# Performance work log

Hardware: AMD Instinct MI355X
Metric: run time of the kernel (lower is better)

The kernel has to match this reference:

```python
import jax, jax.numpy as jnp
import numpy as np

# DeepSeek-MoE-like sizes
T, H, I, E = 4096, 4096, 1408, 16  # tokens, hidden, intermediate, experts
TPE = T // E  # tokens per expert (equal, contiguous groups)


def setup_inputs() -> dict:
    key = jax.random.key(0)
    ks = jax.random.split(key, 5)
    x = jax.random.normal(ks[0], (T, H), dtype=jnp.float32)
    # int8 weights (stored as int8, accumulated in int32)
    w13 = jax.random.randint(ks[1], (E, 2 * I, H), -127, 128, dtype=jnp.int32).astype(jnp.int8)
    w2 = jax.random.randint(ks[2], (E, H, I), -127, 128, dtype=jnp.int32).astype(jnp.int8)
    # per-expert per-output-channel dequant scales (small, realistic magnitudes)
    w13_scale = jax.random.uniform(ks[3], (E, 2 * I), minval=1e-4, maxval=2e-4, dtype=jnp.float32)
    smooth_scale_2 = jnp.ones((E, I), dtype=jnp.float32)
    w2_scale = jax.random.uniform(ks[4], (E, H), minval=1e-4, maxval=2e-4, dtype=jnp.float32)
    # group_list_type=0: cumulative token counts per expert (equal contiguous groups)
    expert_tokens = jnp.cumsum(jnp.full((E,), TPE, dtype=jnp.int32))
    return {"x": x, "w13": w13, "w2": w2, "w13_scale": w13_scale,
            "smooth_scale_2": smooth_scale_2, "w2_scale": w2_scale,
            "expert_tokens": expert_tokens}


def _dynamic_quant(x):
    # per-token symmetric int8 dynamic quantization (npu_dynamic_quant)
    scale = jnp.max(jnp.abs(x), axis=-1, keepdims=True) / 127.0  # [T,1]
    q = jnp.clip(jnp.round(x / scale), -128, 127).astype(jnp.int8)
    return q, scale


def reference(x, w13, w2, w13_scale, smooth_scale_2, w2_scale, expert_tokens):
    # expert_tokens is the cumulative group list; this reference assumes the
    # equal contiguous grouping produced by setup_inputs (TPE tokens/expert).
    del expert_tokens
    # 1) per-token dynamic quant of activations
    xq, s1 = _dynamic_quant(x)                       # int8 [T,H], f32 [T,1]
    xg = xq.reshape(E, TPE, H).astype(jnp.int32)
    s1 = s1.reshape(E, TPE, 1)
    # 2) grouped int8 GEMM -> int32 (w1||w3 fused)
    mm1 = jnp.einsum('eth,eoh->eto', xg, w13.astype(jnp.int32))  # int32 [E,TPE,2I]
    # 3) fused dequant + SwiGLU (activate_left) + smooth-scale + dynamic requant
    y = mm1.astype(jnp.float32) * w13_scale[:, None, :] * s1
    gate, up = y[..., :I], y[..., I:]
    h = jax.nn.silu(gate) * up                        # f32 [E,TPE,I]
    h = h * smooth_scale_2[:, None, :]
    s2 = jnp.max(jnp.abs(h), axis=-1, keepdims=True) / 127.0
    hq = jnp.clip(jnp.round(h / s2), -128, 127).astype(jnp.int32)
    # 4) grouped int8 GEMM with fused per-channel + per-token dequant
    mm2 = jnp.einsum('eti,ehi->eth', hq, w2.astype(jnp.int32))   # int32 [E,TPE,H]
    out = mm2.astype(jnp.float32) * w2_scale[:, None, :] * s2
    return out.reshape(T, H)
```

## Files before the change

### kernel.cpp

```cpp
#include <hip/hip_runtime.h>
#include <stdint.h>

#define T_TOK 4096
#define H_DIM 4096
#define I_DIM 1408
#define E_NUM 16
#define TPE   256

typedef __attribute__((ext_vector_type(4))) int   i32x4;
typedef __attribute__((ext_vector_type(4))) float f32x4;

#define VMCNT(n) asm volatile("s_waitcnt vmcnt(" #n ")" ::: "memory")
#define LGKM0()  asm volatile("s_waitcnt lgkmcnt(0)" ::: "memory")

__device__ __forceinline__ void gload16(const void* g, void* l) {
  __builtin_amdgcn_global_load_lds(
      (const __attribute__((address_space(1))) void*)g,
      (__attribute__((address_space(3))) void*)l, 16, 0, 0);
}

__global__ __launch_bounds__(256)
void quant_x_kernel(const float* __restrict__ x,
                    int8_t* __restrict__ xq,
                    float* __restrict__ s1) {
  const int t   = blockIdx.x;
  const int tid = threadIdx.x;
  const float* row = x + (size_t)t * H_DIM;

  f32x4 v[4];
  float mx = 0.0f;
#pragma unroll
  for (int i = 0; i < 4; ++i) {
    v[i] = *(const f32x4*)(row + (size_t)(i * 256 + tid) * 4);
#pragma unroll
    for (int j = 0; j < 4; ++j) mx = fmaxf(mx, fabsf(v[i][j]));
  }
#pragma unroll
  for (int off = 32; off > 0; off >>= 1) mx = fmaxf(mx, __shfl_xor(mx, off));
  __shared__ float wmax[4];
  if ((tid & 63) == 0) wmax[tid >> 6] = mx;
  __syncthreads();
  float s = fmaxf(fmaxf(wmax[0], wmax[1]), fmaxf(wmax[2], wmax[3])) / 127.0f;
  s = fmaxf(s, 1e-30f);

  int* orow = (int*)(xq + (size_t)t * H_DIM);
#pragma unroll
  for (int i = 0; i < 4; ++i) {
    int packed = 0;
#pragma unroll
    for (int j = 0; j < 4; ++j) {
      float q = rintf(v[i][j] / s);
      q = fminf(fmaxf(q, -128.0f), 127.0f);
      packed |= ((int)q & 0xff) << (8 * j);
    }
    orow[i * 256 + tid] = packed;
  }
  if (tid == 0) s1[t] = s;
}

__global__ __launch_bounds__(256)
void act_quant_kernel(const float* __restrict__ y,
                      const float* __restrict__ smooth,
                      int8_t* __restrict__ hq,
                      float* __restrict__ s2) {
  const int t   = blockIdx.x;
  const int e   = t >> 8;
  const int tid = threadIdx.x;
  const float* gate = y + (size_t)t * (2 * I_DIM);
  const float* up   = gate + I_DIM;
  const float* ss   = smooth + (size_t)e * I_DIM;
  constexpr int NV = I_DIM / 4;

  f32x4 h[2];
  float mx = 0.0f;
#pragma unroll
  for (int i = 0; i < 2; ++i) {
    const int idx = tid + i * 256;
    h[i] = (f32x4)(0.0f);
    if (idx < NV) {
      const f32x4 g4 = *(const f32x4*)(gate + idx * 4);
      const f32x4 u4 = *(const f32x4*)(up + idx * 4);
      const f32x4 s4 = *(const f32x4*)(ss + idx * 4);
#pragma unroll
      for (int j = 0; j < 4; ++j) {
        const float g = g4[j];
        const float sig = 1.0f / (1.0f + expf(-g));
        h[i][j] = ((g * sig) * u4[j]) * s4[j];
        mx = fmaxf(mx, fabsf(h[i][j]));
      }
    }
  }
#pragma unroll
  for (int off = 32; off > 0; off >>= 1) mx = fmaxf(mx, __shfl_xor(mx, off));
  __shared__ float wmax[4];
  if ((tid & 63) == 0) wmax[tid >> 6] = mx;
  __syncthreads();
  float s = fmaxf(fmaxf(wmax[0], wmax[1]), fmaxf(wmax[2], wmax[3])) / 127.0f;
  s = fmaxf(s, 1e-30f);

  int* orow = (int*)(hq + (size_t)t * I_DIM);
#pragma unroll
  for (int i = 0; i < 2; ++i) {
    const int idx = tid + i * 256;
    if (idx < NV) {
      int packed = 0;
#pragma unroll
      for (int j = 0; j < 4; ++j) {
        float q = rintf(h[i][j] / s);
        q = fminf(fmaxf(q, -128.0f), 127.0f);
        packed |= ((int)q & 0xff) << (8 * j);
      }
      orow[idx] = packed;
    }
  }
  if (tid == 0) s2[t] = s;
}

template <int N, int K, int NBLK>
__global__ __launch_bounds__(512, 4)
void gemm_i8_w32_kernel(const int8_t* __restrict__ A,
                        const int* __restrict__ B32,
                        float* __restrict__ C,
                        const float* __restrict__ scaleN,
                        const float* __restrict__ scaleM) {
  constexpr int NT = K / 128;
  __shared__ __align__(16) int8_t As[2][256 * 128];
  __shared__ __align__(16) int8_t Bs[2][64 * 128];

  const int rid  = blockIdx.x;
  const int xcd  = rid & 7;
  const int slot = rid >> 3;
  const int el   = (slot >= NBLK) ? 1 : 0;
  const int e    = 2 * xcd + el;
  const int bn   = slot - el * NBLK;

  const int tid  = threadIdx.x;
  const int lane = tid & 63;
  const int wid  = tid >> 6;
  const int wm   = wid >> 1;
  const int wn   = wid & 1;

  const int8_t* Abase = A + (size_t)e * TPE * K;
  const int*    Bbase = B32 + ((size_t)e * N + (size_t)bn * 64) * (size_t)K;

  const int arow = tid >> 3;
  const int ablk = tid & 7;
  const int akey = arow & 7;
  const int agblk = ablk ^ akey;
  const int8_t* gA[4];
#pragma unroll
  for (int i = 0; i < 4; ++i)
    gA[i] = Abase + (size_t)(arow + 64 * i) * K + (agblk << 4);

  const int brow = tid >> 3;
  const int bblk = tid & 7;
  const int* gB = Bbase + (size_t)brow * K + (bblk << 4);
  const int bldsOff = brow * 128 + ((bblk ^ (brow & 7)) << 4);

  const int r15 = lane & 15;
  const int kg  = lane >> 4;
  int aoff[2][4], boff[2][2];
#pragma unroll
  for (int ks = 0; ks < 2; ++ks) {
#pragma unroll
    for (int m = 0; m < 4; ++m) {
      const int r = wm * 64 + m * 16 + r15;
      aoff[ks][m] = r * 128 + (((ks * 4 + kg) ^ (r & 7)) << 4);
    }
#pragma unroll
    for (int n = 0; n < 2; ++n) {
      const int r = wn * 32 + n * 16 + r15;
      boff[ks][n] = r * 128 + (((ks * 4 + kg) ^ (r & 7)) << 4);
    }
  }

  i32x4 acc[4][2] = {};
  i32x4 n0, n1, n2, n3;

  {
    i32x4 b0 = *(const i32x4*)(gB + 0);
    i32x4 b1 = *(const i32x4*)(gB + 4);
    i32x4 b2 = *(const i32x4*)(gB + 8);
    i32x4 b3 = *(const i32x4*)(gB + 12);
#pragma unroll
    for (int i = 0; i < 4; ++i)
      gload16(gA[i], &As[0][i * 8192 + wid * 1024]);
    VMCNT(4);
    i32x4 pk;
    pk[0] = (b0[0] & 255) | ((b0[1] & 255) << 8) | ((b0[2] & 255) << 16) | (b0[3] << 24);
    pk[1] = (b1[0] & 255) | ((b1[1] & 255) << 8) | ((b1[2] & 255) << 16) | (b1[3] << 24);
    pk[2] = (b2[0] & 255) | ((b2[1] & 255) << 8) | ((b2[2] & 255) << 16) | (b2[3] << 24);
    pk[3] = (b3[0] & 255) | ((b3[1] & 255) << 8) | ((b3[2] & 255) << 16) | (b3[3] << 24);
    *(i32x4*)(&Bs[0][bldsOff]) = pk;
    if (NT > 1) {
      const int* g = gB + 128;
      n0 = *(const i32x4*)(g + 0);
      n1 = *(const i32x4*)(g + 4);
      n2 = *(const i32x4*)(g + 8);
      n3 = *(const i32x4*)(g + 12);
      VMCNT(4);
    } else {
      VMCNT(0);
    }
    LGKM0();
    __builtin_amdgcn_s_barrier();
  }

  for (int t = 0; t < NT; ++t) {
    const int cur = t & 1;
    if (t + 1 < NT) {
      const size_t ko = (size_t)(t + 1) * 128;
#pragma unroll
      for (int i = 0; i < 4; ++i)
        gload16(gA[i] + ko, &As[cur ^ 1][i * 8192 + wid * 1024]);
    }
#pragma unroll
    for (int ks = 0; ks < 2; ++ks) {
      i32x4 av[4], bv[2];
#pragma unroll
      for (int m = 0; m < 4; ++m) av[m] = *(const i32x4*)(&As[cur][aoff[ks][m]]);
#pragma unroll
      for (int n = 0; n < 2; ++n) bv[n] = *(const i32x4*)(&Bs[cur][boff[ks][n]]);
#pragma unroll
      for (int m = 0; m < 4; ++m)
#pragma unroll
        for (int n = 0; n < 2; ++n)
          acc[m][n] = __builtin_amdgcn_mfma_i32_16x16x64_i8(av[m], bv[n], acc[m][n], 0, 0, 0);
    }
    if (t + 1 < NT) {
      VMCNT(4);
      i32x4 pk;
      pk[0] = (n0[0] & 255) | ((n0[1] & 255) << 8) | ((n0[2] & 255) << 16) | (n0[3] << 24);
      pk[1] = (n1[0] & 255) | ((n1[1] & 255) << 8) | ((n1[2] & 255) << 16) | (n1[3] << 24);
      pk[2] = (n2[0] & 255) | ((n2[1] & 255) << 8) | ((n2[2] & 255) << 16) | (n2[3] << 24);
      pk[3] = (n3[0] & 255) | ((n3[1] & 255) << 8) | ((n3[2] & 255) << 16) | (n3[3] << 24);
      *(i32x4*)(&Bs[cur ^ 1][bldsOff]) = pk;
      if (t + 2 < NT) {
        const int* g = gB + (t + 2) * 128;
        n0 = *(const i32x4*)(g + 0);
        n1 = *(const i32x4*)(g + 4);
        n2 = *(const i32x4*)(g + 8);
        n3 = *(const i32x4*)(g + 12);
        VMCNT(4);
      } else {
        VMCNT(0);
      }
      LGKM0();
      __builtin_amdgcn_s_barrier();
    }
  }

  const float* sN = scaleN + (size_t)e * N + (size_t)bn * 64;
  const float* sM = scaleM + e * TPE;
  float* Cbase = C + (size_t)e * TPE * N + (size_t)bn * 64;
#pragma unroll
  for (int m = 0; m < 4; ++m) {
#pragma unroll
    for (int j = 0; j < 4; ++j) {
      const int row = wm * 64 + m * 16 + kg * 4 + j;
      const float smv = sM[row];
      float* cr = Cbase + (size_t)row * N;
#pragma unroll
      for (int n = 0; n < 2; ++n) {
        const int col = wn * 32 + n * 16 + r15;
        cr[col] = ((float)acc[m][n][j] * sN[col]) * smv;
      }
    }
  }
}

extern "C" void kernel_launch(void* const* d_in, const int* in_sizes, int n_in,
                              void* d_out, int out_size, void* d_ws, size_t ws_size,
                              hipStream_t stream) {
  const float* x         = (const float*)d_in[0];
  const int*   w13       = (const int*)d_in[1];
  const int*   w2        = (const int*)d_in[2];
  const float* w13_scale = (const float*)d_in[3];
  const float* smooth    = (const float*)d_in[4];
  const float* w2_scale  = (const float*)d_in[5];

  uint8_t* ws = (uint8_t*)d_ws;
  int8_t* xq = (int8_t*)ws;
  int8_t* hq = (int8_t*)ws;
  float*  s1 = (float*)(ws + 16777216);
  float*  s2 = (float*)(ws + 16777216 + 16384);
  float*  y  = (float*)(ws + 16777216 + 32768);

  float* out = (float*)d_out;

  quant_x_kernel<<<dim3(T_TOK), dim3(256), 0, stream>>>(x, xq, s1);

  gemm_i8_w32_kernel<2 * I_DIM, H_DIM, 44>
      <<<dim3(8 * 2 * 44), dim3(512), 0, stream>>>(
          xq, w13, y, w13_scale, s1);

  act_quant_kernel<<<dim3(T_TOK), dim3(256), 0, stream>>>(y, smooth, hq, s2);

  gemm_i8_w32_kernel<H_DIM, I_DIM, 64>
      <<<dim3(8 * 2 * 64), dim3(512), 0, stream>>>(
          hq, w2, out, w2_scale, s2);
}
```

Measured before the change: 282.8 us.

## Fuse SwiGLU and smooth-scale into GEMM1 epilogue with atomic row max

GEMM1 tiles now pair 32 gate columns with the matching 32 up columns, so the epilogue can dequantize, apply SiLU*up and the smooth scale, and write h (T x I floats) rather than y (T x 2I floats). The per-token absmax is accumulated with a 16-lane shuffle reduction plus an atomicMax on the float bit pattern into a buffer that quant_x_kernel zeroes. A light pack kernel then only quantizes h. This removes half of the intermediate write and read traffic and the separate activation pass, at the cost of global atomics and transcendental work in the GEMM epilogue.

After: 286.4 us. Within noise of the previous version (+1.3%).

```diff
diff --git a/kernel.cpp b/kernel.cpp
--- a/kernel.cpp
+++ b/kernel.cpp
@@ -22,7 +22,8 @@
 __global__ __launch_bounds__(256)
 void quant_x_kernel(const float* __restrict__ x,
                     int8_t* __restrict__ xq,
-                    float* __restrict__ s1) {
+                    float* __restrict__ s1,
+                    unsigned* __restrict__ s2max) {
   const int t   = blockIdx.x;
   const int tid = threadIdx.x;
   const float* row = x + (size_t)t * H_DIM;
@@ -55,84 +56,60 @@
     }
     orow[i * 256 + tid] = packed;
   }
-  if (tid == 0) s1[t] = s;
+  if (tid == 0) { s1[t] = s; s2max[t] = 0u; }
 }
 
 __global__ __launch_bounds__(256)
-void act_quant_kernel(const float* __restrict__ y,
-                      const float* __restrict__ smooth,
-                      int8_t* __restrict__ hq,
-                      float* __restrict__ s2) {
+void act_pack_kernel(const float* __restrict__ h,
+                     const unsigned* __restrict__ s2max,
+                     int8_t* __restrict__ hq,
+                     float* __restrict__ s2) {
   const int t   = blockIdx.x;
-  const int e   = t >> 8;
   const int tid = threadIdx.x;
-  const float* gate = y + (size_t)t * (2 * I_DIM);
-  const float* up   = gate + I_DIM;
-  const float* ss   = smooth + (size_t)e * I_DIM;
   constexpr int NV = I_DIM / 4;
-
-  f32x4 h[2];
-  float mx = 0.0f;
-#pragma unroll
-  for (int i = 0; i < 2; ++i) {
-    const int idx = tid + i * 256;
-    h[i] = (f32x4)(0.0f);
-    if (idx < NV) {
-      const f32x4 g4 = *(const f32x4*)(gate + idx * 4);
-      const f32x4 u4 = *(const f32x4*)(up + idx * 4);
-      const f32x4 s4 = *(const f32x4*)(ss + idx * 4);
-#pragma unroll
-      for (int j = 0; j < 4; ++j) {
-        const float g = g4[j];
-        const float sig = 1.0f / (1.0f + expf(-g));
-        h[i][j] = ((g * sig) * u4[j]) * s4[j];
-        mx = fmaxf(mx, fabsf(h[i][j]));
-      }
-    }
-  }
-#pragma unroll
-  for (int off = 32; off > 0; off >>= 1) mx = fmaxf(mx, __shfl_xor(mx, off));
-  __shared__ float wmax[4];
-  if ((tid & 63) == 0) wmax[tid >> 6] = mx;
-  __syncthreads();
-  float s = fmaxf(fmaxf(wmax[0], wmax[1]), fmaxf(wmax[2], wmax[3])) / 127.0f;
+  float s = __uint_as_float(s2max[t]) / 127.0f;
   s = fmaxf(s, 1e-30f);
-
+  if (tid == 0) s2[t] = s;
+
+  const float* hrow = h + (size_t)t * I_DIM;
   int* orow = (int*)(hq + (size_t)t * I_DIM);
 #pragma unroll
   for (int i = 0; i < 2; ++i) {
     const int idx = tid + i * 256;
     if (idx < NV) {
+      const f32x4 hv = *(const f32x4*)(hrow + idx * 4);
       int packed = 0;
 #pragma unroll
       for (int j = 0; j < 4; ++j) {
-        float q = rintf(h[i][j] / s);
+        float q = rintf(hv[j] / s);
         q = fminf(fmaxf(q, -128.0f), 127.0f);
         packed |= ((int)q & 0xff) << (8 * j);
       }
       orow[idx] = packed;
     }
   }
-  if (tid == 0) s2[t] = s;
-}
-
-template <int N, int K, int NBLK>
+}
+
 __global__ __launch_bounds__(512, 4)
-void gemm_i8_w32_kernel(const int8_t* __restrict__ A,
+void gemm1_fused_kernel(const int8_t* __restrict__ A,
                         const int* __restrict__ B32,
-                        float* __restrict__ C,
-                        const float* __restrict__ scaleN,
-                        const float* __restrict__ scaleM) {
+                        float* __restrict__ Hout,
+                        const float* __restrict__ w13_scale,
+                        const float* __restrict__ smooth,
+                        const float* __restrict__ s1,
+                        unsigned* __restrict__ s2max) {
+  constexpr int K  = H_DIM;
   constexpr int NT = K / 128;
+  constexpr int NPAIR = I_DIM / 32;
   __shared__ __align__(16) int8_t As[2][256 * 128];
-  __shared__ __align__(16) int8_t Bs[2][64 * 128];
+  __shared__ __align__(16) int8_t Bs[2][2 * 32 * 128];
 
   const int rid  = blockIdx.x;
   const int xcd  = rid & 7;
   const int slot = rid >> 3;
-  const int el   = (slot >= NBLK) ? 1 : 0;
+  const int el   = (slot >= NPAIR) ? 1 : 0;
   const int e    = 2 * xcd + el;
-  const int bn   = slot - el * NBLK;
+  const int bn   = slot - el * NPAIR;
 
   const int tid  = threadIdx.x;
   const int lane = tid & 63;
@@ -141,21 +118,23 @@
   const int wn   = wid & 1;
 
   const int8_t* Abase = A + (size_t)e * TPE * K;
-  const int*    Bbase = B32 + ((size_t)e * N + (size_t)bn * 64) * (size_t)K;
+  const int* Bgate = B32 + ((size_t)e * (2 * I_DIM) + (size_t)bn * 32) * (size_t)K;
+  const int* Bup   = Bgate + (size_t)I_DIM * K;
 
   const int arow = tid >> 3;
   const int ablk = tid & 7;
-  const int akey = arow & 7;
-  const int agblk = ablk ^ akey;
+  const int agblk = ablk ^ (arow & 7);
   const int8_t* gA[4];
 #pragma unroll
   for (int i = 0; i < 4; ++i)
     gA[i] = Abase + (size_t)(arow + 64 * i) * K + (agblk << 4);
 
-  const int brow = tid >> 3;
-  const int bblk = tid & 7;
-  const int* gB = Bbase + (size_t)brow * K + (bblk << 4);
-  const int bldsOff = brow * 128 + ((bblk ^ (brow & 7)) << 4);
+  const int btile = tid >> 8;
+  const int bsub  = tid & 255;
+  const int brow  = bsub >> 3;
+  const int bblk  = bsub & 7;
+  const int* gB = (btile ? Bup : Bgate) + (size_t)brow * K + (bblk << 4);
+  const int bldsOff = btile * 4096 + brow * 128 + ((bblk ^ (brow & 7)) << 4);
 
   const int r15 = lane & 15;
   const int kg  = lane >> 4;
@@ -169,8 +148,8 @@
     }
 #pragma unroll
     for (int n = 0; n < 2; ++n) {
-      const int r = wn * 32 + n * 16 + r15;
-      boff[ks][n] = r * 128 + (((ks * 4 + kg) ^ (r & 7)) << 4);
+      const int r = wn * 16 + r15;
+      boff[ks][n] = n * 4096 + r * 128 + (((ks * 4 + kg) ^ (r & 7)) << 4);
     }
   }
 
@@ -192,15 +171,13 @@
     pk[2] = (b2[0] & 255) | ((b2[1] & 255) << 8) | ((b2[2] & 255) << 16) | (b2[3] << 24);
     pk[3] = (b3[0] & 255) | ((b3[1] & 255) << 8) | ((b3[2] & 255) << 16) | (b3[3] << 24);
     *(i32x4*)(&Bs[0][bldsOff]) = pk;
-    if (NT > 1) {
+    {
       const int* g = gB + 128;
       n0 = *(const i32x4*)(g + 0);
       n1 = *(const i32x4*)(g + 4);
       n2 = *(const i32x4*)(g + 8);
       n3 = *(const i32x4*)(g + 12);
       VMCNT(4);
-    } else {
-      VMCNT(0);
     }
     LGKM0();
     __builtin_amdgcn_s_barrier();
@@ -250,6 +227,165 @@
     }
   }
 
+  const int col = bn * 32 + wn * 16 + r15;
+  const float sNg = w13_scale[(size_t)e * (2 * I_DIM) + col];
+  const float sNu = w13_scale[(size_t)e * (2 * I_DIM) + I_DIM + col];
+  const float smo = smooth[(size_t)e * I_DIM + col];
+  const float* s1p = s1 + e * TPE;
+  float* hbase = Hout + (size_t)e * TPE * I_DIM + col;
+  unsigned* s2p = s2max + e * TPE;
+#pragma unroll
+  for (int m = 0; m < 4; ++m) {
+#pragma unroll
+    for (int j = 0; j < 4; ++j) {
+      const int row = wm * 64 + m * 16 + kg * 4 + j;
+      const float s1r = s1p[row];
+      const float g = ((float)acc[m][0][j] * sNg) * s1r;
+      const float u = ((float)acc[m][1][j] * sNu) * s1r;
+      const float sig = 1.0f / (1.0f + expf(-g));
+      const float hv = ((g * sig) * u) * smo;
+      hbase[(size_t)row * I_DIM] = hv;
+      float a = fabsf(hv);
+#pragma unroll
+      for (int d = 1; d < 16; d <<= 1) a = fmaxf(a, __shfl_xor(a, d));
+      if (r15 == 0) atomicMax(&s2p[row], __float_as_uint(a));
+    }
+  }
+}
+
+template <int N, int K, int NBLK>
+__global__ __launch_bounds__(512, 4)
+void gemm_i8_w32_kernel(const int8_t* __restrict__ A,
+                        const int* __restrict__ B32,
+                        float* __restrict__ C,
+                        const float* __restrict__ scaleN,
+                        const float* __restrict__ scaleM) {
+  constexpr int NT = K / 128;
+  __shared__ __align__(16) int8_t As[2][256 * 128];
+  __shared__ __align__(16) int8_t Bs[2][64 * 128];
+
+  const int rid  = blockIdx.x;
+  const int xcd  = rid & 7;
+  const int slot = rid >> 3;
+  const int el   = (slot >= NBLK) ? 1 : 0;
+  const int e    = 2 * xcd + el;
+  const int bn   = slot - el * NBLK;
+
+  const int tid  = threadIdx.x;
+  const int lane = tid & 63;
+  const int wid  = tid >> 6;
+  const int wm   = wid >> 1;
+  const int wn   = wid & 1;
+
+  const int8_t* Abase = A + (size_t)e * TPE * K;
+  const int*    Bbase = B32 + ((size_t)e * N + (size_t)bn * 64) * (size_t)K;
+
+  const int arow = tid >> 3;
+  const int ablk = tid & 7;
+  const int agblk = ablk ^ (arow & 7);
+  const int8_t* gA[4];
+#pragma unroll
+  for (int i = 0; i < 4; ++i)
+    gA[i] = Abase + (size_t)(arow + 64 * i) * K + (agblk << 4);
+
+  const int brow = tid >> 3;
+  const int bblk = tid & 7;
+  const int* gB = Bbase + (size_t)brow * K + (bblk << 4);
+  const int bldsOff = brow * 128 + ((bblk ^ (brow & 7)) << 4);
+
+  const int r15 = lane & 15;
+  const int kg  = lane >> 4;
+  int aoff[2][4], boff[2][2];
+#pragma unroll
+  for (int ks = 0; ks < 2; ++ks) {
+#pragma unroll
+    for (int m = 0; m < 4; ++m) {
+      const int r = wm * 64 + m * 16 + r15;
+      aoff[ks][m] = r * 128 + (((ks * 4 + kg) ^ (r & 7)) << 4);
+    }
+#pragma unroll
+    for (int n = 0; n < 2; ++n) {
+      const int r = wn * 32 + n * 16 + r15;
+      boff[ks][n] = r * 128 + (((ks * 4 + kg) ^ (r & 7)) << 4);
+    }
+  }
+
+  i32x4 acc[4][2] = {};
+  i32x4 n0, n1, n2, n3;
+
+  {
+    i32x4 b0 = *(const i32x4*)(gB + 0);
+    i32x4 b1 = *(const i32x4*)(gB + 4);
+    i32x4 b2 = *(const i32x4*)(gB + 8);
+    i32x4 b3 = *(const i32x4*)(gB + 12);
+#pragma unroll
+    for (int i = 0; i < 4; ++i)
+      gload16(gA[i], &As[0][i * 8192 + wid * 1024]);
+    VMCNT(4);
+    i32x4 pk;
+    pk[0] = (b0[0] & 255) | ((b0[1] & 255) << 8) | ((b0[2] & 255) << 16) | (b0[3] << 24);
+    pk[1] = (b1[0] & 255) | ((b1[1] & 255) << 8) | ((b1[2] & 255) << 16) | (b1[3] << 24);
+    pk[2] = (b2[0] & 255) | ((b2[1] & 255) << 8) | ((b2[2] & 255) << 16) | (b2[3] << 24);
+    pk[3] = (b3[0] & 255) | ((b3[1] & 255) << 8) | ((b3[2] & 255) << 16) | (b3[3] << 24);
+    *(i32x4*)(&Bs[0][bldsOff]) = pk;
+    if (NT > 1) {
+      const int* g = gB + 128;
+      n0 = *(const i32x4*)(g + 0);
+      n1 = *(const i32x4*)(g + 4);
+      n2 = *(const i32x4*)(g + 8);
+      n3 = *(const i32x4*)(g + 12);
+      VMCNT(4);
+    } else {
+      VMCNT(0);
+    }
+    LGKM0();
+    __builtin_amdgcn_s_barrier();
+  }
+
+  for (int t = 0; t < NT; ++t) {
+    const int cur = t & 1;
+    if (t + 1 < NT) {
+      const size_t ko = (size_t)(t + 1) * 128;
+#pragma unroll
+      for (int i = 0; i < 4; ++i)
+        gload16(gA[i] + ko, &As[cur ^ 1][i * 8192 + wid * 1024]);
+    }
+#pragma unroll
+    for (int ks = 0; ks < 2; ++ks) {
+      i32x4 av[4], bv[2];
+#pragma unroll
+      for (int m = 0; m < 4; ++m) av[m] = *(const i32x4*)(&As[cur][aoff[ks][m]]);
+#pragma unroll
+      for (int n = 0; n < 2; ++n) bv[n] = *(const i32x4*)(&Bs[cur][boff[ks][n]]);
+#pragma unroll
+      for (int m = 0; m < 4; ++m)
+#pragma unroll
+        for (int n = 0; n < 2; ++n)
+          acc[m][n] = __builtin_amdgcn_mfma_i32_16x16x64_i8(av[m], bv[n], acc[m][n], 0, 0, 0);
+    }
+    if (t + 1 < NT) {
+      VMCNT(4);
+      i32x4 pk;
+      pk[0] = (n0[0] & 255) | ((n0[1] & 255) << 8) | ((n0[2] & 255) << 16) | (n0[3] << 24);
+      pk[1] = (n1[0] & 255) | ((n1[1] & 255) << 8) | ((n1[2] & 255) << 16) | (n1[3] << 24);
+      pk[2] = (n2[0] & 255) | ((n2[1] & 255) << 8) | ((n2[2] & 255) << 16) | (n2[3] << 24);
+      pk[3] = (n3[0] & 255) | ((n3[1] & 255) << 8) | ((n3[2] & 255) << 16) | (n3[3] << 24);
+      *(i32x4*)(&Bs[cur ^ 1][bldsOff]) = pk;
+      if (t + 2 < NT) {
+        const int* g = gB + (t + 2) * 128;
+        n0 = *(const i32x4*)(g + 0);
+        n1 = *(const i32x4*)(g + 4);
+        n2 = *(const i32x4*)(g + 8);
+        n3 = *(const i32x4*)(g + 12);
+        VMCNT(4);
+      } else {
+        VMCNT(0);
+      }
+      LGKM0();
+      __builtin_amdgcn_s_barrier();
+    }
+  }
+
   const float* sN = scaleN + (size_t)e * N + (size_t)bn * 64;
   const float* sM = scaleM + e * TPE;
   float* Cbase = C + (size_t)e * TPE * N + (size_t)bn * 64;
@@ -280,21 +416,21 @@
   const float* w2_scale  = (const float*)d_in[5];
 
   uint8_t* ws = (uint8_t*)d_ws;
-  int8_t* xq = (int8_t*)ws;
-  int8_t* hq = (int8_t*)ws;
-  float*  s1 = (float*)(ws + 16777216);
-  float*  s2 = (float*)(ws + 16777216 + 16384);
-  float*  y  = (float*)(ws + 16777216 + 32768);
+  int8_t*   xq    = (int8_t*)ws;
+  int8_t*   hq    = (int8_t*)ws;
+  float*    s1    = (float*)(ws + 16777216);
+  float*    s2    = (float*)(ws + 16777216 + 16384);
+  unsigned* s2max = (unsigned*)(ws + 16777216 + 32768);
+  float*    h     = (float*)(ws + 16777216 + 49152);
 
   float* out = (float*)d_out;
 
-  quant_x_kernel<<<dim3(T_TOK), dim3(256), 0, stream>>>(x, xq, s1);
-
-  gemm_i8_w32_kernel<2 * I_DIM, H_DIM, 44>
-      <<<dim3(8 * 2 * 44), dim3(512), 0, stream>>>(
-          xq, w13, y, w13_scale, s1);
-
-  act_quant_kernel<<<dim3(T_TOK), dim3(256), 0, stream>>>(y, smooth, hq, s2);
+  quant_x_kernel<<<dim3(T_TOK), dim3(256), 0, stream>>>(x, xq, s1, s2max);
+
+  gemm1_fused_kernel<<<dim3(8 * 2 * (I_DIM / 32)), dim3(512), 0, stream>>>(
+      xq, w13, h, w13_scale, smooth, s1, s2max);
+
+  act_pack_kernel<<<dim3(T_TOK), dim3(256), 0, stream>>>(h, s2max, hq, s2);
 
   gemm_i8_w32_kernel<H_DIM, I_DIM, 64>
       <<<dim3(8 * 2 * 64), dim3(512), 0, stream>>>(
```
